# Performance work log

Hardware: AMD Instinct MI355X
Metric: run time of the kernel (lower is better)

## Reference

```python
import jax, jax.numpy as jnp
import numpy as np

N = 100000   # nodes
E = 1600000  # edges
D = 128      # hidden_dim (also input feature dim)
R = 8        # num_relations
B = 4        # num_bases
OUT = 64     # out_dim
P = 2        # gating exponent p


def setup_inputs() -> dict:
    key = jax.random.key(0)
    ks = jax.random.split(key, 16)
    w = lambda k, shape, s=0.05: jax.random.normal(k, shape, dtype=jnp.float32) * s
    return {
        "x": jax.random.normal(ks[0], (N, D), dtype=jnp.float32),
        "src": jax.random.randint(ks[1], (E,), 0, N, dtype=jnp.int32),
        "dst": jax.random.randint(ks[2], (E,), 0, N, dtype=jnp.int32),
        "edge_type": jax.random.randint(ks[3], (E,), 0, R, dtype=jnp.int32),
        "proj_W": w(ks[4], (D, D)), "proj_b": jnp.zeros((D,), jnp.float32),
        "basis1": w(ks[5], (B, D, D)), "comp1": w(ks[6], (R, B), 1.0),
        "root1": w(ks[7], (D, D)), "bias1": jnp.zeros((D,), jnp.float32),
        "basis2": w(ks[8], (B, D, D)), "comp2": w(ks[9], (R, B), 1.0),
        "root2": w(ks[10], (D, D)), "bias2": jnp.zeros((D,), jnp.float32),
        "out_W": w(ks[11], (D, OUT)), "out_b": jnp.zeros((OUT,), jnp.float32),
    }


def _rgcn(x, src, dst, et, basis, comp, root, bias):
    # PyG RGCNConv (basis decomposition, aggr='mean'):
    # out_i = x_i @ root + bias + sum_r mean_{e: dst=i, type=r}( x_{src_e} @ W_r )
    # Mean is linear, so aggregate raw features per (node, relation), then matmul.
    n, d = x.shape
    seg = dst * R + et                                   # combined (node, relation) key
    agg = jax.ops.segment_sum(x[src], seg, num_segments=n * R).reshape(n, R, d)
    cnt = jax.ops.segment_sum(jnp.ones(seg.shape, x.dtype), seg, num_segments=n * R).reshape(n, R)
    agg = agg / jnp.maximum(cnt, 1.0)[:, :, None]        # empty segments -> 0
    W = jnp.einsum('rb,bdf->rdf', comp, basis)           # [R, D, D] relation weights
    return jnp.einsum('nrd,rdf->nf', agg, W) + x @ root + bias


def _gate(x, src, dst):
    # tau = tanh(scatter_mean(|x_src - x_dst|^p, index=src))
    diff = jnp.abs(x[src] - x[dst]) ** P                 # [E, D]
    s = jax.ops.segment_sum(diff, src, num_segments=x.shape[0])
    c = jax.ops.segment_sum(jnp.ones(src.shape, x.dtype), src, num_segments=x.shape[0])
    return jnp.tanh(s / jnp.maximum(c, 1.0)[:, None])


def reference(x, src, dst, edge_type, proj_W, proj_b,
              basis1, comp1, root1, bias1,
              basis2, comp2, root2, bias2,
              out_W, out_b):
    # input projection (dropout is identity in eval mode)
    h = jax.nn.relu(x @ proj_W + proj_b)
    latents = [h]
    for basis, comp, root, bias in ((basis1, comp1, root1, bias1),
                                    (basis2, comp2, root2, bias2)):
        h_new = jax.nn.relu(_rgcn(h, src, dst, edge_type, basis, comp, root, bias))
        tau = _gate(h, src, dst)
        h = (1.0 - tau) * h + tau * h_new
        latents.append(h)
    out = h @ out_W + out_b
    return (out, jnp.stack(latents))
```

## Files before the change

kernel.cpp:

```cpp
#include <hip/hip_runtime.h>
#include <cstdint>
#include <cstddef>

#define D 128
#define RR 8

typedef __attribute__((ext_vector_type(8))) short short8;
typedef __attribute__((ext_vector_type(4))) float f32x4;

__device__ inline ushort f2b(float x) {
    union { float f; unsigned u; } v; v.f = x;
    unsigned r = v.u + 0x7fff + ((v.u >> 16) & 1);
    return (ushort)(r >> 16);
}
__device__ inline float b2f(ushort u) {
    union { unsigned u; float f; } v; v.u = ((unsigned)u) << 16; return v.f;
}

__device__ inline void gload_lds16(const ushort* g, ushort* l) {
    __builtin_amdgcn_global_load_lds(
        (const __attribute__((address_space(1))) unsigned int*)g,
        (__attribute__((address_space(3))) unsigned int*)l, 16, 0, 0);
}

template<bool BIAS, bool RELU, bool STF, bool STB, bool GATE>
__global__ __launch_bounds__(256, 4) void gemm_bf16(
    const ushort* __restrict__ A0, int lda0, int k0steps,
    const ushort* __restrict__ A1, int lda1,
    const ushort* __restrict__ BT, int ktiles,
    const float* __restrict__ bias, float* __restrict__ Cf, int ldcf,
    ushort* __restrict__ Cb, int ldcb,
    const float* __restrict__ hp, const ushort* __restrict__ TAU,
    int M, int ncol)
{
    __shared__ ushort As[128 * 64];
    __shared__ ushort Bs[128 * 64];
    const int tid = threadIdx.x;
    const int m0 = blockIdx.x * 128;
    const int ldb = ktiles * 128;
    const int ksteps = ktiles * 2;

    const int w = tid >> 6, lane = tid & 63;
    const int wm = (w & 1) * 64, wn = (w >> 1) * 64;
    const int l15 = lane & 15, quad = lane >> 4;

    const ushort* a0p[4];
    const ushort* a1p[4];
    const ushort* bp[4];
#pragma unroll
    for (int it = 0; it < 4; it++) {
        int gi = w * 256 + it * 64 + lane;
        int row = gi >> 3, g = gi & 7;
        int cg = g ^ (row & 7);
        int gr = m0 + row; if (gr > M - 1) gr = M - 1;
        a0p[it] = A0 + (size_t)gr * lda0 + (cg << 3);
        a1p[it] = A1 + (size_t)gr * lda1 + (cg << 3);
        bp[it]  = BT + (size_t)row * ldb + (cg << 3);
    }

    f32x4 acc[4][4];
    const f32x4 z4 = {0.f, 0.f, 0.f, 0.f};
#pragma unroll
    for (int i = 0; i < 4; i++)
#pragma unroll
        for (int j = 0; j < 4; j++) acc[i][j] = z4;

    for (int kt = 0; kt < ksteps; kt++) {
        const int ko = kt * 64;
        if (kt < k0steps) {
#pragma unroll
            for (int it = 0; it < 4; it++)
                gload_lds16(a0p[it] + ko, As + w * 2048 + it * 512);
        } else {
            const int ko1 = (kt - k0steps) * 64;
#pragma unroll
            for (int it = 0; it < 4; it++)
                gload_lds16(a1p[it] + ko1, As + w * 2048 + it * 512);
        }
#pragma unroll
        for (int it = 0; it < 4; it++)
            gload_lds16(bp[it] + ko, Bs + w * 2048 + it * 512);
        __syncthreads();

#pragma unroll
        for (int ks = 0; ks < 64; ks += 32) {
            const int q0 = (ks >> 3) + quad;
            short8 af[4], bfr[4];
#pragma unroll
            for (int i = 0; i < 4; i++) {
                int row = wm + i * 16 + l15;
                af[i] = *(const short8*)(&As[row * 64 + ((q0 ^ (row & 7)) << 3)]);
            }
#pragma unroll
            for (int j = 0; j < 4; j++) {
                int row = wn + j * 16 + l15;
                bfr[j] = *(const short8*)(&Bs[row * 64 + ((q0 ^ (row & 7)) << 3)]);
            }
#pragma unroll
            for (int i = 0; i < 4; i++)
#pragma unroll
                for (int j = 0; j < 4; j++)
                    acc[i][j] = __builtin_amdgcn_mfma_f32_16x16x32_bf16(
                        af[i], bfr[j], acc[i][j], 0, 0, 0);
        }
        __syncthreads();
    }

#pragma unroll
    for (int i = 0; i < 4; i++) {
#pragma unroll
        for (int q = 0; q < 4; q++) {
            int gm = m0 + wm + i * 16 + quad * 4 + q;
            if (gm >= M) continue;
#pragma unroll
            for (int j = 0; j < 4; j++) {
                int gn = wn + j * 16 + l15;
                if (gn >= ncol) continue;
                float v = acc[i][j][q];
                if (BIAS) v += bias[gn];
                if (RELU) v = v > 0.f ? v : 0.f;
                if (GATE) {
                    float pv  = hp[(size_t)gm * 128 + gn];
                    float tau = b2f(TAU[(size_t)gm * 128 + gn]);
                    v = pv + tau * (v - pv);
                }
                if (STF) Cf[(size_t)gm * ldcf + gn] = v;
                if (STB) Cb[(size_t)gm * ldcb + gn] = f2b(v);
            }
        }
    }
}

__global__ void build_bigBT(const float* __restrict__ basis,
                            const float* __restrict__ comp,
                            const float* __restrict__ root,
                            ushort* __restrict__ BT)
{
    int i = blockIdx.x * 256 + threadIdx.x;
    if (i >= 128 * 1152) return;
    int f = i / 1152, c = i - f * 1152;
    float a;
    if (c < 1024) {
        int r = c >> 7, d = c & 127;
        a = 0.f;
#pragma unroll
        for (int b = 0; b < 4; b++)
            a += comp[r * 4 + b] * basis[(b * 128 + d) * 128 + f];
    } else {
        a = root[(c - 1024) * 128 + f];
    }
    BT[i] = f2b(a);
}

__global__ void transpose_pad(const float* __restrict__ in, ushort* __restrict__ out,
                              int cols)
{
    int i = blockIdx.x * 256 + threadIdx.x;
    if (i >= 128 * 128) return;
    int k = i & 127, f = i >> 7;
    out[i] = (f < cols) ? f2b(in[k * cols + f]) : (ushort)0;
}

__global__ void cast_x(const float* __restrict__ in, ushort* __restrict__ Hc, int total4)
{
    int i = blockIdx.x * 256 + threadIdx.x;
    if (i >= total4) return;
    float4 v = ((const float4*)in)[i];
    ushort4 o = { f2b(v.x), f2b(v.y), f2b(v.z), f2b(v.w) };
    *(ushort4*)(Hc + (size_t)i * 4) = o;
}

__global__ void count_slot(const int* __restrict__ src, const int* __restrict__ dst,
                           const int* __restrict__ et, int* __restrict__ cnt,
                           int* __restrict__ deg, int* __restrict__ slotA,
                           int* __restrict__ slotG, int E)
{
    int t = blockIdx.x * 256 + threadIdx.x;
    int e0 = t * 4;
    if (e0 + 4 <= E) {
        int4 s4 = ((const int4*)src)[t];
        int4 d4 = ((const int4*)dst)[t];
        int4 t4 = ((const int4*)et)[t];
        int4 sa, sg;
        sa.x = atomicAdd(&cnt[d4.x * RR + t4.x], 1);
        sa.y = atomicAdd(&cnt[d4.y * RR + t4.y], 1);
        sa.z = atomicAdd(&cnt[d4.z * RR + t4.z], 1);
        sa.w = atomicAdd(&cnt[d4.w * RR + t4.w], 1);
        sg.x = atomicAdd(&deg[s4.x], 1);
        sg.y = atomicAdd(&deg[s4.y], 1);
        sg.z = atomicAdd(&deg[s4.z], 1);
        sg.w = atomicAdd(&deg[s4.w], 1);
        ((int4*)slotA)[t] = sa;
        ((int4*)slotG)[t] = sg;
    } else {
        for (int e = e0; e < E; e++) {
            slotA[e] = atomicAdd(&cnt[dst[e] * RR + et[e]], 1);
            slotG[e] = atomicAdd(&deg[src[e]], 1);
        }
    }
}

__global__ void scan1(const int* __restrict__ in, int* __restrict__ bsum, int n)
{
    __shared__ int s[256];
    const int b = blockIdx.x, t = threadIdx.x;
    const int base = b * 1024;
    int v = 0;
#pragma unroll
    for (int i = 0; i < 4; i++) {
        int idx = base + t * 4 + i;
        if (idx < n) v += in[idx];
    }
    s[t] = v; __syncthreads();
    for (int off = 128; off > 0; off >>= 1) {
        if (t < off) s[t] += s[t + off];
        __syncthreads();
    }
    if (t == 0) bsum[b] = s[0];
}

__global__ void scan_top(int* __restrict__ bsum, int nb)
{
    __shared__ int s[1024];
    const int t = threadIdx.x;
    int v = (t < nb) ? bsum[t] : 0;
    s[t] = v; __syncthreads();
    for (int off = 1; off < 1024; off <<= 1) {
        int x = (t >= off) ? s[t - off] : 0;
        __syncthreads();
        s[t] += x;
        __syncthreads();
    }
    if (t < nb) bsum[t] = s[t] - v;
}

__global__ void scan2(const int* __restrict__ in, const int* __restrict__ bsum,
                      int* __restrict__ out, int n)
{
    __shared__ int s[256];
    const int b = blockIdx.x, t = threadIdx.x;
    const int base = b * 1024;
    int loc[4];
    int v = 0;
#pragma unroll
    for (int i = 0; i < 4; i++) {
        int idx = base + t * 4 + i;
        int x = (idx < n) ? in[idx] : 0;
        loc[i] = v; v += x;
    }
    s[t] = v; __syncthreads();
    for (int off = 1; off < 256; off <<= 1) {
        int x = (t >= off) ? s[t - off] : 0;
        __syncthreads();
        s[t] += x;
        __syncthreads();
    }
    const int add = bsum[b] + (s[t] - v);
#pragma unroll
    for (int i = 0; i < 4; i++) {
        int idx = base + t * 4 + i;
        if (idx < n) out[idx] = add + loc[i];
    }
}

__global__ void fill_scatter(const int* __restrict__ src, const int* __restrict__ dst,
                             const int* __restrict__ et,
                             const int* __restrict__ aoff, const int* __restrict__ goff,
                             const int* __restrict__ slotA, const int* __restrict__ slotG,
                             int* __restrict__ acsr, int* __restrict__ gcsr, int E)
{
    int t = blockIdx.x * 256 + threadIdx.x;
    int e0 = t * 4;
    if (e0 + 4 <= E) {
        int4 s4 = ((const int4*)src)[t];
        int4 d4 = ((const int4*)dst)[t];
        int4 t4 = ((const int4*)et)[t];
        int4 sa = ((const int4*)slotA)[t];
        int4 sg = ((const int4*)slotG)[t];
        acsr[aoff[d4.x * RR + t4.x] + sa.x] = s4.x;
        acsr[aoff[d4.y * RR + t4.y] + sa.y] = s4.y;
        acsr[aoff[d4.z * RR + t4.z] + sa.z] = s4.z;
        acsr[aoff[d4.w * RR + t4.w] + sa.w] = s4.w;
        gcsr[goff[s4.x] + sg.x] = d4.x;
        gcsr[goff[s4.y] + sg.y] = d4.y;
        gcsr[goff[s4.z] + sg.z] = d4.z;
        gcsr[goff[s4.w] + sg.w] = d4.w;
    } else {
        for (int e = e0; e < E; e++) {
            int s0 = src[e], d0 = dst[e];
            acsr[aoff[d0 * RR + et[e]] + slotA[e]] = s0;
            gcsr[goff[s0] + slotG[e]] = d0;
        }
    }
}

__global__ __launch_bounds__(256) void gathers(
    ushort* __restrict__ Agg, const ushort* __restrict__ Hc,
    const int* __restrict__ acsr, const int* __restrict__ aoff,
    const int* __restrict__ cnt,
    const int* __restrict__ gcsr, const int* __restrict__ goff,
    const int* __restrict__ deg, ushort* __restrict__ TAUb,
    int N, int nbA)
{
    const int g = threadIdx.x >> 4, lane = threadIdx.x & 15;
    if (blockIdx.x < nbA) {
        const int n = blockIdx.x * 16 + g;
        if (n >= N) return;
        const int sbase = n * RR;
        const int start = aoff[sbase];
        int ctot = 0;
#pragma unroll
        for (int r0 = 0; r0 < RR; r0++) ctot += cnt[sbase + r0];

        const ushort* hbase = Hc + lane * 8;
        ushort* obase = Agg + (size_t)n * 1024 + lane * 8;

        float cum[8];
#pragma unroll
        for (int j = 0; j < 8; j++) cum[j] = 0.f;
        int r = 0;
        int segstart = 0;
        int nexte = cnt[sbase];

        auto flush = [&]() {
            int c = nexte - segstart;
            short8 outv = {0, 0, 0, 0, 0, 0, 0, 0};
            if (c > 0) {
                float inv = 1.f / (float)c;
#pragma unroll
                for (int j = 0; j < 8; j++) outv[j] = (short)f2b(cum[j] * inv);
            }
            __builtin_nontemporal_store(outv, (short8*)(obase + r * 128));
#pragma unroll
            for (int j = 0; j < 8; j++) cum[j] = 0.f;
            segstart = nexte;
            r++;
            if (r < RR) nexte += cnt[sbase + r];
        };

        int i = 0;
        for (; i + 4 <= ctot; i += 4) {
            int s0 = acsr[start + i],     s1 = acsr[start + i + 1];
            int s2 = acsr[start + i + 2], s3 = acsr[start + i + 3];
            short8 y0 = *(const short8*)(hbase + (size_t)s0 * 128);
            short8 y1 = *(const short8*)(hbase + (size_t)s1 * 128);
            short8 y2 = *(const short8*)(hbase + (size_t)s2 * 128);
            short8 y3 = *(const short8*)(hbase + (size_t)s3 * 128);
            while (i >= nexte) flush();
#pragma unroll
            for (int j = 0; j < 8; j++) cum[j] += b2f((ushort)y0[j]);
            while (i + 1 >= nexte) flush();
#pragma unroll
            for (int j = 0; j < 8; j++) cum[j] += b2f((ushort)y1[j]);
            while (i + 2 >= nexte) flush();
#pragma unroll
            for (int j = 0; j < 8; j++) cum[j] += b2f((ushort)y2[j]);
            while (i + 3 >= nexte) flush();
#pragma unroll
            for (int j = 0; j < 8; j++) cum[j] += b2f((ushort)y3[j]);
        }
        for (; i < ctot; i++) {
            int s0 = acsr[start + i];
            short8 y0 = *(const short8*)(hbase + (size_t)s0 * 128);
            while (i >= nexte) flush();
#pragma unroll
            for (int j = 0; j < 8; j++) cum[j] += b2f((ushort)y0[j]);
        }
        while (r < RR) flush();
    } else {
        const int n = (blockIdx.x - nbA) * 16 + g;
        if (n >= N) return;
        const int start = goff[n];
        const int c = deg[n];
        const ushort* hbase = Hc + lane * 8;
        const short8 a8 = *(const short8*)(hbase + (size_t)n * 128);
        float av[8];
#pragma unroll
        for (int j = 0; j < 8; j++) av[j] = b2f((ushort)a8[j]);
        float acc[8];
#pragma unroll
        for (int j = 0; j < 8; j++) acc[j] = 0.f;

        int i = 0;
        for (; i + 4 <= c; i += 4) {
            int d0 = gcsr[start + i],     d1 = gcsr[start + i + 1];
            int d2 = gcsr[start + i + 2], d3 = gcsr[start + i + 3];
            short8 b0 = *(const short8*)(hbase + (size_t)d0 * 128);
            short8 b1 = *(const short8*)(hbase + (size_t)d1 * 128);
            short8 b2 = *(const short8*)(hbase + (size_t)d2 * 128);
            short8 b3 = *(const short8*)(hbase + (size_t)d3 * 128);
#pragma unroll
            for (int j = 0; j < 8; j++) {
                float dx0 = av[j] - b2f((ushort)b0[j]);
                float dx1 = av[j] - b2f((ushort)b1[j]);
                float dx2 = av[j] - b2f((ushort)b2[j]);
                float dx3 = av[j] - b2f((ushort)b3[j]);
                acc[j] += dx0 * dx0 + dx1 * dx1 + dx2 * dx2 + dx3 * dx3;
            }
        }
        if (i + 2 <= c) {
            int d0 = gcsr[start + i], d1 = gcsr[start + i + 1];
            short8 b0 = *(const short8*)(hbase + (size_t)d0 * 128);
            short8 b1 = *(const short8*)(hbase + (size_t)d1 * 128);
#pragma unroll
            for (int j = 0; j < 8; j++) {
                float dx0 = av[j] - b2f((ushort)b0[j]);
                float dx1 = av[j] - b2f((ushort)b1[j]);
                acc[j] += dx0 * dx0 + dx1 * dx1;
            }
            i += 2;
        }
        if (i < c) {
            int d0 = gcsr[start + i];
            short8 b0 = *(const short8*)(hbase + (size_t)d0 * 128);
#pragma unroll
            for (int j = 0; j < 8; j++) {
                float dx0 = av[j] - b2f((ushort)b0[j]);
                acc[j] += dx0 * dx0;
            }
        }
        const float inv = (c > 0) ? (1.f / (float)c) : 1.f;
        short8 t;
#pragma unroll
        for (int j = 0; j < 8; j++) t[j] = (short)f2b(tanhf(acc[j] * inv));
        *(short8*)(TAUb + (size_t)n * D + lane * 8) = t;
    }
}

extern "C" void kernel_launch(void* const* d_in, const int* in_sizes, int n_in,
                              void* d_out, int out_size, void* d_ws, size_t ws_size,
                              hipStream_t stream)
{
    const float* x      = (const float*)d_in[0];
    const int*   src    = (const int*)  d_in[1];
    const int*   dst    = (const int*)  d_in[2];
    const int*   etyp   = (const int*)  d_in[3];
    const float* projW  = (const float*)d_in[4];
    const float* projb  = (const float*)d_in[5];
    const float* basis1 = (const float*)d_in[6];
    const float* comp1  = (const float*)d_in[7];
    const float* root1  = (const float*)d_in[8];
    const float* bias1  = (const float*)d_in[9];
    const float* basis2 = (const float*)d_in[10];
    const float* comp2  = (const float*)d_in[11];
    const float* root2  = (const float*)d_in[12];
    const float* bias2  = (const float*)d_in[13];
    const float* outW   = (const float*)d_in[14];
    const float* outb   = (const float*)d_in[15];

    const int N    = in_sizes[0] / D;
    const int E    = in_sizes[1];
    const int OUTD = in_sizes[15];

    float* out  = (float*)d_out;
    float* lat0 = out + (size_t)N * OUTD;
    float* lat1 = lat0 + (size_t)N * D;
    float* lat2 = lat1 + (size_t)N * D;

    char* p = (char*)d_ws;
    ushort* Agg   = (ushort*)p;  p += (size_t)N * 1024 * 2;
    ushort* Hc    = (ushort*)p;  p += (size_t)N * 128 * 2;
    ushort* TAUb  = (ushort*)p;  p += (size_t)N * D * 2;
    ushort* projWT = (ushort*)p; p += 16384 * 2;
    ushort* outWT  = (ushort*)p; p += 16384 * 2;
    ushort* bigBT1 = (ushort*)p; p += (size_t)128 * 1152 * 2;
    ushort* bigBT2 = (ushort*)p; p += (size_t)128 * 1152 * 2;
    int* cnt_i  = (int*)p;       p += (size_t)N * RR * 4;
    int* deg_i  = (int*)p;       p += (size_t)N * 4;
    int* aoff   = (int*)p;       p += (size_t)N * RR * 4;
    int* goff   = (int*)p;       p += (size_t)N * 4;
    int* slotA  = (int*)p;       p += (size_t)E * 4;
    int* slotG  = (int*)p;       p += (size_t)E * 4;
    int* acsr   = (int*)p;       p += (size_t)E * 4;
    int* gcsr   = (int*)p;       p += (size_t)E * 4;
    int* bsum   = (int*)p;       p += 4096;

    if ((size_t)(p - (char*)d_ws) > ws_size) return;

    hipMemsetAsync(cnt_i, 0, sizeof(int) * ((size_t)N * RR + N), stream);

    build_bigBT<<<(128 * 1152 + 255) / 256, 256, 0, stream>>>(basis1, comp1, root1, bigBT1);
    build_bigBT<<<(128 * 1152 + 255) / 256, 256, 0, stream>>>(basis2, comp2, root2, bigBT2);
    transpose_pad<<<64, 256, 0, stream>>>(projW, projWT, 128);
    transpose_pad<<<64, 256, 0, stream>>>(outW, outWT, OUTD);

    cast_x<<<(N * 32 + 255) / 256, 256, 0, stream>>>(x, Hc, N * 32);

    count_slot<<<(E / 4 + 255) / 256, 256, 0, stream>>>(
        src, dst, etyp, cnt_i, deg_i, slotA, slotG, E);

    {
        int n1 = N * RR, nb1 = (n1 + 1023) / 1024;
        scan1<<<nb1, 256, 0, stream>>>(cnt_i, bsum, n1);
        scan_top<<<1, 1024, 0, stream>>>(bsum, nb1);
        scan2<<<nb1, 256, 0, stream>>>(cnt_i, bsum, aoff, n1);
        int nb2 = (N + 1023) / 1024;
        scan1<<<nb2, 256, 0, stream>>>(deg_i, bsum, N);
        scan_top<<<1, 1024, 0, stream>>>(bsum, nb2);
        scan2<<<nb2, 256, 0, stream>>>(deg_i, bsum, goff, N);
    }

    fill_scatter<<<(E / 4 + 255) / 256, 256, 0, stream>>>(
        src, dst, etyp, aoff, goff, slotA, slotG, acsr, gcsr, E);

    const int mb = (N + 127) / 128;
    const int nbA = (N + 15) / 16;

    gemm_bf16<true, true, true, true, false><<<mb, 256, 0, stream>>>(
        Hc, 128, 2, Hc, 128, projWT, 1, projb, lat0, 128, Hc, 128,
        nullptr, nullptr, N, 128);

    const ushort* bigBT[2] = {bigBT1, bigBT2};
    const float* biases[2] = {bias1, bias2};
    float* lats[3]         = {lat0, lat1, lat2};

    for (int l = 0; l < 2; l++) {
        float* hn = lats[l + 1];

        gathers<<<2 * nbA, 256, 0, stream>>>(
            Agg, Hc, acsr, aoff, cnt_i, gcsr, goff, deg_i, TAUb, N, nbA);

        gemm_bf16<true, true, true, true, true><<<mb, 256, 0, stream>>>(
            Agg, 1024, 16, Hc, 128, bigBT[l], 9, biases[l], hn, 128, Hc, 128,
            lats[l], TAUb, N, 128);
    }

    gemm_bf16<true, false, true, false, false><<<mb, 256, 0, stream>>>(
        Hc, 128, 2, Hc, 128, outWT, 1, outb, out, OUTD, nullptr, 0,
        nullptr, nullptr, N, OUTD);
}
```

Before: 998.2 us.

## Merge prep, projection+count, and scan kernels into fewer launches

Folds the weight-prep kernels and the x cast into one prep launch. It runs the input projection GEMM and the edge counting in one launch by splitting on block index, and batches the two prefix scans into paired kernels. This cuts launch count and serial dependencies so independent work can share the GPU. The risk is that heterogeneous blocks share launch bounds and LDS allocation, which may hurt occupancy for the counting blocks.

Result: no change. 979.1 us (-1.9%).

```diff
diff --git a/kernel.cpp b/kernel.cpp
--- a/kernel.cpp
+++ b/kernel.cpp
@@ -24,7 +24,8 @@
 }
 
 template<bool BIAS, bool RELU, bool STF, bool STB, bool GATE>
-__global__ __launch_bounds__(256, 4) void gemm_bf16(
+__device__ inline void gemm_body(
+    ushort* As, ushort* Bs, int blk,
     const ushort* __restrict__ A0, int lda0, int k0steps,
     const ushort* __restrict__ A1, int lda1,
     const ushort* __restrict__ BT, int ktiles,
@@ -33,10 +34,8 @@
     const float* __restrict__ hp, const ushort* __restrict__ TAU,
     int M, int ncol)
 {
-    __shared__ ushort As[128 * 64];
-    __shared__ ushort Bs[128 * 64];
     const int tid = threadIdx.x;
-    const int m0 = blockIdx.x * 128;
+    const int m0 = blk * 128;
     const int ldb = ktiles * 128;
     const int ksteps = ktiles * 2;
 
@@ -131,51 +130,29 @@
     }
 }
 
-__global__ void build_bigBT(const float* __restrict__ basis,
-                            const float* __restrict__ comp,
-                            const float* __restrict__ root,
-                            ushort* __restrict__ BT)
-{
-    int i = blockIdx.x * 256 + threadIdx.x;
-    if (i >= 128 * 1152) return;
-    int f = i / 1152, c = i - f * 1152;
-    float a;
-    if (c < 1024) {
-        int r = c >> 7, d = c & 127;
-        a = 0.f;
-#pragma unroll
-        for (int b = 0; b < 4; b++)
-            a += comp[r * 4 + b] * basis[(b * 128 + d) * 128 + f];
-    } else {
-        a = root[(c - 1024) * 128 + f];
-    }
-    BT[i] = f2b(a);
-}
-
-__global__ void transpose_pad(const float* __restrict__ in, ushort* __restrict__ out,
-                              int cols)
-{
-    int i = blockIdx.x * 256 + threadIdx.x;
-    if (i >= 128 * 128) return;
-    int k = i & 127, f = i >> 7;
-    out[i] = (f < cols) ? f2b(in[k * cols + f]) : (ushort)0;
-}
-
-__global__ void cast_x(const float* __restrict__ in, ushort* __restrict__ Hc, int total4)
-{
-    int i = blockIdx.x * 256 + threadIdx.x;
-    if (i >= total4) return;
-    float4 v = ((const float4*)in)[i];
-    ushort4 o = { f2b(v.x), f2b(v.y), f2b(v.z), f2b(v.w) };
-    *(ushort4*)(Hc + (size_t)i * 4) = o;
-}
-
-__global__ void count_slot(const int* __restrict__ src, const int* __restrict__ dst,
-                           const int* __restrict__ et, int* __restrict__ cnt,
-                           int* __restrict__ deg, int* __restrict__ slotA,
-                           int* __restrict__ slotG, int E)
-{
-    int t = blockIdx.x * 256 + threadIdx.x;
+template<bool BIAS, bool RELU, bool STF, bool STB, bool GATE>
+__global__ __launch_bounds__(256, 4) void gemm_bf16(
+    const ushort* __restrict__ A0, int lda0, int k0steps,
+    const ushort* __restrict__ A1, int lda1,
+    const ushort* __restrict__ BT, int ktiles,
+    const float* __restrict__ bias, float* __restrict__ Cf, int ldcf,
+    ushort* __restrict__ Cb, int ldcb,
+    const float* __restrict__ hp, const ushort* __restrict__ TAU,
+    int M, int ncol)
+{
+    __shared__ ushort As[128 * 64];
+    __shared__ ushort Bs[128 * 64];
+    gemm_body<BIAS, RELU, STF, STB, GATE>(As, Bs, blockIdx.x,
+        A0, lda0, k0steps, A1, lda1, BT, ktiles, bias, Cf, ldcf,
+        Cb, ldcb, hp, TAU, M, ncol);
+}
+
+__device__ inline void count_body(
+    const int* __restrict__ src, const int* __restrict__ dst,
+    const int* __restrict__ et, int* __restrict__ cnt,
+    int* __restrict__ deg, int* __restrict__ slotA,
+    int* __restrict__ slotG, int E, int t)
+{
     int e0 = t * 4;
     if (e0 + 4 <= E) {
         int4 s4 = ((const int4*)src)[t];
@@ -200,10 +177,86 @@
     }
 }
 
-__global__ void scan1(const int* __restrict__ in, int* __restrict__ bsum, int n)
-{
-    __shared__ int s[256];
-    const int b = blockIdx.x, t = threadIdx.x;
+__global__ __launch_bounds__(256, 4) void proj_count(
+    ushort* __restrict__ Hc, const ushort* __restrict__ projWT,
+    const float* __restrict__ projb, float* __restrict__ lat0, int M,
+    const int* __restrict__ src, const int* __restrict__ dst,
+    const int* __restrict__ et, int* __restrict__ cnt, int* __restrict__ deg,
+    int* __restrict__ slotA, int* __restrict__ slotG, int E, int mb)
+{
+    __shared__ ushort As[128 * 64];
+    __shared__ ushort Bs[128 * 64];
+    if ((int)blockIdx.x < mb) {
+        gemm_body<true, true, true, true, false>(As, Bs, blockIdx.x,
+            Hc, 128, 2, Hc, 128, projWT, 1, projb, lat0, 128, Hc, 128,
+            nullptr, nullptr, M, 128);
+    } else {
+        count_body(src, dst, et, cnt, deg, slotA, slotG, E,
+                   (blockIdx.x - mb) * 256 + threadIdx.x);
+    }
+}
+
+__device__ inline void bigBT_body(const float* __restrict__ basis,
+                                  const float* __restrict__ comp,
+                                  const float* __restrict__ root,
+                                  ushort* __restrict__ BT, int i)
+{
+    if (i >= 128 * 1152) return;
+    int f = i / 1152, c = i - f * 1152;
+    float a;
+    if (c < 1024) {
+        int r = c >> 7, d = c & 127;
+        a = 0.f;
+#pragma unroll
+        for (int b = 0; b < 4; b++)
+            a += comp[r * 4 + b] * basis[(b * 128 + d) * 128 + f];
+    } else {
+        a = root[(c - 1024) * 128 + f];
+    }
+    BT[i] = f2b(a);
+}
+
+__device__ inline void transpose_body(const float* __restrict__ in,
+                                      ushort* __restrict__ out, int cols, int i)
+{
+    if (i >= 128 * 128) return;
+    int k = i & 127, f = i >> 7;
+    out[i] = (f < cols) ? f2b(in[k * cols + f]) : (ushort)0;
+}
+
+__global__ void prep(
+    const float* __restrict__ x, ushort* __restrict__ Hc, int total4, int nbCast,
+    const float* __restrict__ basis1, const float* __restrict__ comp1,
+    const float* __restrict__ root1, ushort* __restrict__ BT1,
+    const float* __restrict__ basis2, const float* __restrict__ comp2,
+    const float* __restrict__ root2, ushort* __restrict__ BT2, int nbBig,
+    const float* __restrict__ projW, ushort* __restrict__ projWT,
+    const float* __restrict__ outW, ushort* __restrict__ outWT, int OUTD)
+{
+    int b = blockIdx.x, tid = threadIdx.x;
+    if (b < nbCast) {
+        int i = b * 256 + tid;
+        if (i < total4) {
+            float4 v = ((const float4*)x)[i];
+            ushort4 o = { f2b(v.x), f2b(v.y), f2b(v.z), f2b(v.w) };
+            *(ushort4*)(Hc + (size_t)i * 4) = o;
+        }
+        return;
+    }
+    b -= nbCast;
+    if (b < nbBig) { bigBT_body(basis1, comp1, root1, BT1, b * 256 + tid); return; }
+    b -= nbBig;
+    if (b < nbBig) { bigBT_body(basis2, comp2, root2, BT2, b * 256 + tid); return; }
+    b -= nbBig;
+    if (b < 64) { transpose_body(projW, projWT, 128, b * 256 + tid); return; }
+    b -= 64;
+    transpose_body(outW, outWT, OUTD, b * 256 + tid);
+}
+
+__device__ inline void scan1_body(int* s, const int* __restrict__ in,
+                                  int* __restrict__ bsum, int n, int b)
+{
+    const int t = threadIdx.x;
     const int base = b * 1024;
     int v = 0;
 #pragma unroll
@@ -219,9 +272,50 @@
     if (t == 0) bsum[b] = s[0];
 }
 
-__global__ void scan_top(int* __restrict__ bsum, int nb)
+__device__ inline void scan2_body(int* s, const int* __restrict__ in,
+                                  const int* __restrict__ bsum,
+                                  int* __restrict__ out, int n, int b)
+{
+    const int t = threadIdx.x;
+    const int base = b * 1024;
+    int loc[4];
+    int v = 0;
+#pragma unroll
+    for (int i = 0; i < 4; i++) {
+        int idx = base + t * 4 + i;
+        int x = (idx < n) ? in[idx] : 0;
+        loc[i] = v; v += x;
+    }
+    s[t] = v; __syncthreads();
+    for (int off = 1; off < 256; off <<= 1) {
+        int x = (t >= off) ? s[t - off] : 0;
+        __syncthreads();
+        s[t] += x;
+        __syncthreads();
+    }
+    const int add = bsum[b] + (s[t] - v);
+#pragma unroll
+    for (int i = 0; i < 4; i++) {
+        int idx = base + t * 4 + i;
+        if (idx < n) out[idx] = add + loc[i];
+    }
+}
+
+__global__ void scan1m(const int* __restrict__ inA, int* __restrict__ bsumA,
+                       int nA, int nbA,
+                       const int* __restrict__ inG, int* __restrict__ bsumG, int nG)
+{
+    __shared__ int s[256];
+    if ((int)blockIdx.x < nbA) scan1_body(s, inA, bsumA, nA, blockIdx.x);
+    else                       scan1_body(s, inG, bsumG, nG, blockIdx.x - nbA);
+}
+
+__global__ void scan_top2(int* __restrict__ bsumA, int nb1,
+                          int* __restrict__ bsumG, int nb2)
 {
     __shared__ int s[1024];
+    int* bsum = (blockIdx.x == 0) ? bsumA : bsumG;
+    int nb    = (blockIdx.x == 0) ? nb1 : nb2;
     const int t = threadIdx.x;
     int v = (t < nb) ? bsum[t] : 0;
     s[t] = v; __syncthreads();
@@ -234,33 +328,14 @@
     if (t < nb) bsum[t] = s[t] - v;
 }
 
-__global__ void scan2(const int* __restrict__ in, const int* __restrict__ bsum,
-                      int* __restrict__ out, int n)
+__global__ void scan2m(const int* __restrict__ inA, const int* __restrict__ bsumA,
+                       int* __restrict__ outA, int nA, int nbA,
+                       const int* __restrict__ inG, const int* __restrict__ bsumG,
+                       int* __restrict__ outG, int nG)
 {
     __shared__ int s[256];
-    const int b = blockIdx.x, t = threadIdx.x;
-    const int base = b * 1024;
-    int loc[4];
-    int v = 0;
-#pragma unroll
-    for (int i = 0; i < 4; i++) {
-        int idx = base + t * 4 + i;
-        int x = (idx < n) ? in[idx] : 0;
-        loc[i] = v; v += x;
-    }
-    s[t] = v; __syncthreads();
-    for (int off = 1; off < 256; off <<= 1) {
-        int x = (t >= off) ? s[t - off] : 0;
-        __syncthreads();
-        s[t] += x;
-        __syncthreads();
-    }
-    const int add = bsum[b] + (s[t] - v);
-#pragma unroll
-    for (int i = 0; i < 4; i++) {
-        int idx = base + t * 4 + i;
-        if (idx < n) out[idx] = add + loc[i];
-    }
+    if ((int)blockIdx.x < nbA) scan2_body(s, inA, bsumA, outA, nA, blockIdx.x);
+    else                       scan2_body(s, inG, bsumG, outG, nG, blockIdx.x - nbA);
 }
 
 __global__ void fill_scatter(const int* __restrict__ src, const int* __restrict__ dst,
@@ -303,7 +378,7 @@
     int N, int nbA)
 {
     const int g = threadIdx.x >> 4, lane = threadIdx.x & 15;
-    if (blockIdx.x < nbA) {
+    if ((int)blockIdx.x < nbA) {
         const int n = blockIdx.x * 16 + g;
         if (n >= N) return;
         const int sbase = n * RR;
@@ -473,42 +548,40 @@
     int* slotG  = (int*)p;       p += (size_t)E * 4;
     int* acsr   = (int*)p;       p += (size_t)E * 4;
     int* gcsr   = (int*)p;       p += (size_t)E * 4;
-    int* bsum   = (int*)p;       p += 4096;
+    int* bsumA  = (int*)p;       p += 4096;
+    int* bsumG  = (int*)p;       p += 4096;
 
     if ((size_t)(p - (char*)d_ws) > ws_size) return;
 
     hipMemsetAsync(cnt_i, 0, sizeof(int) * ((size_t)N * RR + N), stream);
 
-    build_bigBT<<<(128 * 1152 + 255) / 256, 256, 0, stream>>>(basis1, comp1, root1, bigBT1);
-    build_bigBT<<<(128 * 1152 + 255) / 256, 256, 0, stream>>>(basis2, comp2, root2, bigBT2);
-    transpose_pad<<<64, 256, 0, stream>>>(projW, projWT, 128);
-    transpose_pad<<<64, 256, 0, stream>>>(outW, outWT, OUTD);
-
-    cast_x<<<(N * 32 + 255) / 256, 256, 0, stream>>>(x, Hc, N * 32);
-
-    count_slot<<<(E / 4 + 255) / 256, 256, 0, stream>>>(
-        src, dst, etyp, cnt_i, deg_i, slotA, slotG, E);
+    const int mb  = (N + 127) / 128;
+    const int nbA = (N + 15) / 16;
+    const int nbCast = (N * 32 + 255) / 256;
+    const int nbBig  = (128 * 1152 + 255) / 256;
+    const int cb  = (E / 4 + 255) / 256;
+
+    prep<<<nbCast + 2 * nbBig + 64 + 64, 256, 0, stream>>>(
+        x, Hc, N * 32, nbCast,
+        basis1, comp1, root1, bigBT1,
+        basis2, comp2, root2, bigBT2, nbBig,
+        projW, projWT, outW, outWT, OUTD);
+
+    proj_count<<<mb + cb, 256, 0, stream>>>(
+        Hc, projWT, projb, lat0, N,
+        src, dst, etyp, cnt_i, deg_i, slotA, slotG, E, mb);
 
     {
         int n1 = N * RR, nb1 = (n1 + 1023) / 1024;
-        scan1<<<nb1, 256, 0, stream>>>(cnt_i, bsum, n1);
-        scan_top<<<1, 1024, 0, stream>>>(bsum, nb1);
-        scan2<<<nb1, 256, 0, stream>>>(cnt_i, bsum, aoff, n1);
         int nb2 = (N + 1023) / 1024;
-        scan1<<<nb2, 256, 0, stream>>>(deg_i, bsum, N);
-        scan_top<<<1, 1024, 0, stream>>>(bsum, nb2);
-        scan2<<<nb2, 256, 0, stream>>>(deg_i, bsum, goff, N);
-    }
-
-    fill_scatter<<<(E / 4 + 255) / 256, 256, 0, stream>>>(
+        scan1m<<<nb1 + nb2, 256, 0, stream>>>(cnt_i, bsumA, n1, nb1, deg_i, bsumG, N);
+        scan_top2<<<2, 1024, 0, stream>>>(bsumA, nb1, bsumG, nb2);
+        scan2m<<<nb1 + nb2, 256, 0, stream>>>(cnt_i, bsumA, aoff, n1, nb1,
+                                              deg_i, bsumG, goff, N);
+    }
+
+    fill_scatter<<<cb, 256, 0, stream>>>(
         src, dst, etyp, aoff, goff, slotA, slotG, acsr, gcsr, E);
-
-    const int mb = (N + 127) / 128;
-    const int nbA = (N + 15) / 16;
-
-    gemm_bf16<true, true, true, true, false><<<mb, 256, 0, stream>>>(
-        Hc, 128, 2, Hc, 128, projWT, 1, projb, lat0, 128, Hc, 128,
-        nullptr, nullptr, N, 128);
 
     const ushort* bigBT[2] = {bigBT1, bigBT2};
     const float* biases[2] = {bias1, bias2};
```
